# Kernel tuning notes

Hardware: AMD Instinct MI355X
Metric: run time of the kernel (lower is better)

Reference implementation:

```python
import jax, jax.numpy as jnp
import numpy as np
import math

DIM_V = 512
NUM_HEADS = 8
LN_EPS = 1e-5


def _layer_norm(x, g, b):
    mu = jnp.mean(x, axis=-1, keepdims=True)
    var = jnp.mean(jnp.square(x - mu), axis=-1, keepdims=True)
    return (x - mu) * jax.lax.rsqrt(var + LN_EPS) * g + b


def setup_inputs() -> dict:
    key = jax.random.key(0)
    ks = jax.random.split(key, 12)
    B, Nq, Nk, Dq, Dk, Dv = 16, 1024, 1024, 512, 512, DIM_V
    s_q = 1.0 / math.sqrt(Dq)
    s_k = 1.0 / math.sqrt(Dk)
    s_v = 1.0 / math.sqrt(Dv)
    return {
        "Q": jax.random.normal(ks[0], (B, Nq, Dq), jnp.float32),
        "K": jax.random.normal(ks[1], (B, Nk, Dk), jnp.float32),
        "Wq": jax.random.normal(ks[2], (Dq, Dv), jnp.float32) * s_q,
        "bq": jnp.zeros((Dv,), jnp.float32),
        "Wk": jax.random.normal(ks[3], (Dk, Dv), jnp.float32) * s_k,
        "bk": jnp.zeros((Dv,), jnp.float32),
        "Wv": jax.random.normal(ks[4], (Dk, Dv), jnp.float32) * s_k,
        "bv": jnp.zeros((Dv,), jnp.float32),
        "Wo": jax.random.normal(ks[5], (Dv, Dv), jnp.float32) * s_v,
        "bo": jnp.zeros((Dv,), jnp.float32),
        "g0": jnp.ones((Dv,), jnp.float32),
        "b0": jnp.zeros((Dv,), jnp.float32),
        "g1": jnp.ones((Dv,), jnp.float32),
        "b1": jnp.zeros((Dv,), jnp.float32),
    }


def reference(Q, K, Wq, bq, Wk, bk, Wv, bv, Wo, bo, g0, b0, g1, b1):
    B, Nq, _ = Q.shape
    H = NUM_HEADS
    hd = DIM_V // H
    Qp = Q @ Wq + bq            # [B, Nq, Dv]
    Kp = K @ Wk + bk            # [B, Nk, Dv]
    Vp = K @ Wv + bv            # [B, Nk, Dv]
    # split heads: [B, N, H, hd]
    Qh = Qp.reshape(B, Nq, H, hd)
    Kh = Kp.reshape(B, -1, H, hd)
    Vh = Vp.reshape(B, -1, H, hd)
    # NOTE: original scales by sqrt(dim_V), not sqrt(head_dim)
    scores = jnp.einsum("bqhd,bkhd->bhqk", Qh, Kh) / math.sqrt(DIM_V)
    A = jax.nn.softmax(scores, axis=-1)          # [B, H, Nq, Nk]
    Oh = Qh + jnp.einsum("bhqk,bkhd->bqhd", A, Vh)  # residual on projected Q
    O = Oh.reshape(B, Nq, DIM_V)
    O = _layer_norm(O, g0, b0)
    O = O + jax.nn.relu(O @ Wo + bo)
    O = _layer_norm(O, g1, b1)
    return O
```

## Files before the change

### kernel.cpp

```cpp
#include <hip/hip_runtime.h>
#include <hip/hip_bf16.h>

typedef float f32x4 __attribute__((ext_vector_type(4)));
typedef float f32x16 __attribute__((ext_vector_type(16)));
typedef __bf16 bf16x8 __attribute__((ext_vector_type(8)));
typedef __bf16 bf16x4 __attribute__((ext_vector_type(4)));

#define MFMA(a, b, c) __builtin_amdgcn_mfma_f32_16x16x32_bf16(a, b, c, 0, 0, 0)
#define MFMA32(a, b, c) __builtin_amdgcn_mfma_f32_32x32x16_bf16(a, b, c, 0, 0, 0)
#define AS1 __attribute__((address_space(1)))
#define AS3 __attribute__((address_space(3)))

__device__ __forceinline__ void gload16(const void* g, void* l) {
    __builtin_amdgcn_global_load_lds((const AS1 unsigned int*)g, (AS3 unsigned int*)l, 16, 0, 0);
}

__device__ __forceinline__ unsigned short f2bf(float f) {
    union { float f; unsigned u; } x{f};
    unsigned r = x.u + 0x7FFFu + ((x.u >> 16) & 1u);
    return (unsigned short)(r >> 16);
}
__device__ __forceinline__ float bf2f(unsigned short u) {
    union { unsigned u; float f; } x; x.u = ((unsigned)u) << 16; return x.f;
}
__device__ __forceinline__ unsigned pkbf(float a, float b) {
    union { __bf16 h[2]; unsigned u; } r;
    r.h[0] = (__bf16)a; r.h[1] = (__bf16)b;
    return r.u;
}

__device__ __forceinline__ void softmax_pack(const f32x16& s0, const f32x16& s1,
                                             float& ls, int hi, bf16x8* pf) {
    unsigned We[8], Wf[8];
    #pragma unroll
    for (int g = 0; g < 4; ++g) {
        float e0 = __builtin_amdgcn_exp2f(s0[4 * g + 0]);
        float e1 = __builtin_amdgcn_exp2f(s0[4 * g + 1]);
        float e2 = __builtin_amdgcn_exp2f(s0[4 * g + 2]);
        float e3 = __builtin_amdgcn_exp2f(s0[4 * g + 3]);
        float f0 = __builtin_amdgcn_exp2f(s1[4 * g + 0]);
        float f1 = __builtin_amdgcn_exp2f(s1[4 * g + 1]);
        float f2 = __builtin_amdgcn_exp2f(s1[4 * g + 2]);
        float f3 = __builtin_amdgcn_exp2f(s1[4 * g + 3]);
        ls += ((e0 + e1) + (e2 + e3)) + ((f0 + f1) + (f2 + f3));
        We[2 * g + 0] = pkbf(e0, e1); We[2 * g + 1] = pkbf(e2, e3);
        Wf[2 * g + 0] = pkbf(f0, f1); Wf[2 * g + 1] = pkbf(f2, f3);
    }
    #pragma unroll
    for (int src = 0; src < 2; ++src) {
        const unsigned* W = src == 0 ? We : Wf;
        #pragma unroll
        for (int k2 = 0; k2 < 2; ++k2) {
            unsigned A0 = W[4 * k2 + 0], A1 = W[4 * k2 + 1];
            unsigned B0 = W[4 * k2 + 2], B1 = W[4 * k2 + 3];
            unsigned cross0 = __shfl_xor(hi ? A0 : B0, 32);
            unsigned cross1 = __shfl_xor(hi ? A1 : B1, 32);
            union { unsigned w[4]; bf16x8 v; } r;
            r.w[0] = hi ? cross0 : A0;
            r.w[1] = hi ? cross1 : A1;
            r.w[2] = hi ? B0 : cross0;
            r.w[3] = hi ? B1 : cross1;
            pf[src * 2 + k2] = r.v;
        }
    }
}

__global__ __launch_bounds__(256) void k_pack4(const float* W0, const float* W1,
                                               const float* W2, const float* W3,
                                               unsigned short* P0, unsigned short* P1,
                                               unsigned short* P2, unsigned short* P3) {
    __shared__ float T[64][65];
    int sel = blockIdx.x >> 6, tile = blockIdx.x & 63;
    const float* W = sel == 0 ? W0 : sel == 1 ? W1 : sel == 2 ? W2 : W3;
    unsigned short* Wp = sel == 0 ? P0 : sel == 1 ? P1 : sel == 2 ? P2 : P3;
    int k0 = (tile >> 3) * 64, n0 = (tile & 7) * 64;
    int tid = threadIdx.x;
    for (int it = 0; it < 16; ++it) {
        int id = it * 256 + tid;
        int r = id >> 6, c = id & 63;
        T[r][c] = W[(k0 + r) * 512 + n0 + c];
    }
    __syncthreads();
    if (sel < 3) {
        #pragma unroll
        for (int cc = 0; cc < 2; ++cc) {
            int ch = cc * 256 + tid;
            int ksl = ch >> 8, n16l = (ch >> 6) & 3, ln = ch & 63;
            int kg = ln >> 4, nl = ln & 15;
            union { unsigned short u[8]; int4 v; } tmp;
            #pragma unroll
            for (int e = 0; e < 8; ++e)
                tmp.u[e] = f2bf(T[ksl * 32 + kg * 8 + e][n16l * 16 + nl]);
            size_t dst = ((size_t)((k0 >> 5) + ksl) * 32 + (n0 >> 4) + n16l) * 512 + ln * 8;
            *(int4*)(Wp + dst) = tmp.v;
        }
    } else {
        for (int it = 0; it < 16; ++it) {
            int id = it * 256 + tid;
            int r = id >> 6, c = id & 63;
            Wp[(n0 + r) * 512 + k0 + c] = f2bf(T[c][r]);
        }
    }
}

__global__ __launch_bounds__(512, 4) void k_proj3(const float* __restrict__ Qf,
                                                  const float* __restrict__ Kf,
                                                  const unsigned short* __restrict__ WpQ,
                                                  const unsigned short* __restrict__ WpK,
                                                  const unsigned short* __restrict__ WpV,
                                                  const float* __restrict__ bq,
                                                  const float* __restrict__ bk,
                                                  const float* __restrict__ bv,
                                                  unsigned short* __restrict__ Qsc,
                                                  unsigned short* __restrict__ Kp,
                                                  unsigned short* __restrict__ VpT,
                                                  float scale2) {
    __shared__ __align__(16) unsigned short Asm[2][2048];
    const int tid = threadIdx.x, lane = tid & 63, w = tid >> 6;
    const int l15 = lane & 15, l4 = lane >> 4;
    const int bid = blockIdx.x;
    const int sel = bid >> 8, rt = bid & 255;
    const float* A = sel == 0 ? Qf : Kf;
    const unsigned short* Wp = sel == 0 ? WpQ : sel == 1 ? WpK : WpV;
    const int m0 = rt * 64;
    const int wn = w * 64;

    const f32x4 vz = {0.f, 0.f, 0.f, 0.f};
    f32x4 acc[4][4];
    for (int i = 0; i < 4; ++i)
        for (int j = 0; j < 4; ++j) acc[i][j] = vz;

    const int sr = tid >> 3, sc4 = tid & 7;
    const float* aptr = A + (size_t)(m0 + sr) * 512 + sc4 * 4;
    unsigned short* const wdst =
        &Asm[0][0] + sr * 32 + ((sc4 >> 1) ^ (sr & 3)) * 8 + (sc4 & 1) * 4;

    auto WRITEA = [&](const float4& v, int p) {
        union { unsigned u[2]; } r;
        r.u[0] = pkbf(v.x, v.y);
        r.u[1] = pkbf(v.z, v.w);
        *(uint2*)(wdst + p * 2048) = *(uint2*)&r;
    };

    {
        float4 a0 = *(const float4*)(aptr);
        WRITEA(a0, 0);
    }
    __syncthreads();

    const unsigned short* wbase = Wp + (size_t)(w * 4) * 512 + lane * 8;
    if (sel < 2) {
        for (int ks = 0; ks < 16; ++ks) {
            int p = ks & 1;
            float4 anx;
            if (ks < 15) anx = *(const float4*)(aptr + (ks + 1) * 32);
            bf16x8 bfr[4], afr[4];
            #pragma unroll
            for (int j = 0; j < 4; ++j)
                bfr[j] = *(const bf16x8*)(wbase + (size_t)ks * 16384 + j * 512);
            #pragma unroll
            for (int i = 0; i < 4; ++i) {
                int rr = i * 16 + l15;
                afr[i] = *(const bf16x8*)&Asm[p][rr * 32 + (l4 ^ (rr & 3)) * 8];
            }
            __builtin_amdgcn_s_setprio(1);
            #pragma unroll
            for (int i = 0; i < 4; ++i)
                #pragma unroll
                for (int j = 0; j < 4; ++j)
                    acc[i][j] = MFMA(afr[i], bfr[j], acc[i][j]);
            __builtin_amdgcn_s_setprio(0);
            if (ks < 15) WRITEA(anx, p ^ 1);
            __syncthreads();
        }
        const float* bias = sel ? bk : bq;
        unsigned short* out = sel ? Kp : Qsc;
        const float scale = sel ? 1.0f : scale2;
        float bn[4];
        #pragma unroll
        for (int j = 0; j < 4; ++j) bn[j] = bias[wn + j * 16 + l15];
        for (int i = 0; i < 4; ++i)
            for (int j = 0; j < 4; ++j)
                for (int rg = 0; rg < 4; ++rg) {
                    int m = m0 + i * 16 + l4 * 4 + rg;
                    int n = wn + j * 16 + l15;
                    out[(size_t)m * 512 + n] = f2bf((acc[i][j][rg] + bn[j]) * scale);
                }
    } else {
        for (int ks = 0; ks < 16; ++ks) {
            int p = ks & 1;
            float4 anx;
            if (ks < 15) anx = *(const float4*)(aptr + (ks + 1) * 32);
            bf16x8 bfr[4], afr[4];
            #pragma unroll
            for (int j = 0; j < 4; ++j)
                bfr[j] = *(const bf16x8*)(wbase + (size_t)ks * 16384 + j * 512);
            #pragma unroll
            for (int i = 0; i < 4; ++i) {
                int rr = i * 16 + l15;
                afr[i] = *(const bf16x8*)&Asm[p][rr * 32 + (l4 ^ (rr & 3)) * 8];
            }
            __builtin_amdgcn_s_setprio(1);
            #pragma unroll
            for (int i = 0; i < 4; ++i)
                #pragma unroll
                for (int j = 0; j < 4; ++j)
                    acc[i][j] = MFMA(bfr[j], afr[i], acc[i][j]);
            __builtin_amdgcn_s_setprio(0);
            if (ks < 15) WRITEA(anx, p ^ 1);
            __syncthreads();
        }
        const int b = m0 >> 10, key0 = m0 & 1023;
        for (int j = 0; j < 4; ++j) {
            float4 bv4 = *(const float4*)(bv + wn + j * 16 + l4 * 4);
            for (int i = 0; i < 4; ++i)
                for (int rg = 0; rg < 4; ++rg) {
                    int d = wn + j * 16 + l4 * 4 + rg;
                    int key = key0 + i * 16 + l15;
                    VpT[((size_t)(b * 512 + d)) * 1024 + key] = f2bf(acc[i][j][rg] + bv4[rg]);
                }
        }
    }
}

__global__ __launch_bounds__(128, 2) void k_attn64(const unsigned short* __restrict__ Qs,
                                                   const unsigned short* __restrict__ Kp,
                                                   const unsigned short* __restrict__ VpT,
                                                   unsigned short* __restrict__ O1b) {
    __shared__ __align__(16) unsigned short sm[16384];
    const int tid = threadIdx.x, lane = tid & 63, w = tid >> 6;
    const int l31 = lane & 31, hi = lane >> 5;
    int i = blockIdx.x;
    const int xcd = i & 7, r2 = i >> 3;
    const int bhl = r2 & 15, qt = r2 >> 4;
    const int bh = xcd * 16 + bhl;
    const int h = bh & 7, b = bh >> 3;
    const int q0 = b * 1024 + qt * 128 + w * 64;
    const int kv0 = (qt * 3 + bhl * 5) & 15;

    const unsigned short* Ksrc = Kp + (size_t)(b * 1024) * 512 + h * 64;
    const unsigned short* Vsrc = VpT + (size_t)(b * 512 + h * 64) * 1024;
    const unsigned short* qptrA = Qs + (size_t)(q0 + l31) * 512 + h * 64;
    const unsigned short* qptrB = qptrA + (size_t)32 * 512;

    bf16x8 qfA[4], qfB[4];
    #pragma unroll
    for (int ks = 0; ks < 4; ++ks) {
        qfA[ks] = *(const bf16x8*)(qptrA + ks * 16 + hi * 8);
        qfB[ks] = *(const bf16x8*)(qptrB + ks * 16 + hi * 8);
    }

    f32x16 accA0, accA1, accB0, accB1;
    #pragma unroll
    for (int r = 0; r < 16; ++r) { accA0[r] = 0.f; accA1[r] = 0.f; accB0[r] = 0.f; accB1[r] = 0.f; }
    float lsA = 0.f, lsB = 0.f;

    auto STAGE = [&](int j, int p) {
        int t = (j + kv0) & 15;
        #pragma unroll
        for (int it = 0; it < 4; ++it) {
            int id = it * 128 + tid;
            int r = id >> 3, x = id & 7, c = x ^ (r & 7);
            unsigned short* kb = sm + p * 4096 + (it * 128 + w * 64) * 8;
            gload16(Ksrc + (size_t)(t * 64 + r) * 512 + c * 8, kb);
            gload16(Vsrc + (size_t)r * 1024 + t * 64 + c * 8, kb + 8192);
        }
    };

    STAGE(0, 0);
    __syncthreads();
    const int rsw = l31 & 7;
    for (int it2 = 0; it2 < 16; ++it2) {
        int p = it2 & 1;
        if (it2 < 15) STAGE(it2 + 1, p ^ 1);
        const unsigned short* Kl = sm + p * 4096;
        const unsigned short* Vl = sm + 8192 + p * 4096;

        f32x16 s0a, s1a, s0b, s1b;
        #pragma unroll
        for (int r = 0; r < 16; ++r) { s0a[r] = 0.f; s1a[r] = 0.f; s0b[r] = 0.f; s1b[r] = 0.f; }
        __builtin_amdgcn_s_setprio(1);
        #pragma unroll
        for (int ks = 0; ks < 4; ++ks) {
            int c = (2 * ks + hi) ^ rsw;
            bf16x8 kf0 = *(const bf16x8*)&Kl[l31 * 64 + c * 8];
            bf16x8 kf1 = *(const bf16x8*)&Kl[(32 + l31) * 64 + c * 8];
            s0a = MFMA32(kf0, qfA[ks], s0a);
            s1a = MFMA32(kf1, qfA[ks], s1a);
            s0b = MFMA32(kf0, qfB[ks], s0b);
            s1b = MFMA32(kf1, qfB[ks], s1b);
        }
        __builtin_amdgcn_s_setprio(0);

        bf16x8 pfA[4], pfB[4];
        softmax_pack(s0a, s1a, lsA, hi, pfA);
        softmax_pack(s0b, s1b, lsB, hi, pfB);

        __builtin_amdgcn_s_setprio(1);
        #pragma unroll
        for (int ks = 0; ks < 4; ++ks) {
            int c = (2 * ks + hi) ^ rsw;
            bf16x8 vf0 = *(const bf16x8*)&Vl[l31 * 64 + c * 8];
            bf16x8 vf1 = *(const bf16x8*)&Vl[(32 + l31) * 64 + c * 8];
            accA0 = MFMA32(vf0, pfA[ks], accA0);
            accA1 = MFMA32(vf1, pfA[ks], accA1);
            accB0 = MFMA32(vf0, pfB[ks], accB0);
            accB1 = MFMA32(vf1, pfB[ks], accB1);
        }
        __builtin_amdgcn_s_setprio(0);
        __syncthreads();
    }

    const float invscale = 15.6841306f;
    {
        float l = lsA + __shfl_xor(lsA, 32);
        float linv = 1.0f / l;
        unsigned short* orow = O1b + (size_t)(q0 + l31) * 512 + h * 64;
        #pragma unroll
        for (int g = 0; g < 4; ++g) {
            int d0 = 8 * g + 4 * hi;
            bf16x4 qres = *(const bf16x4*)(qptrA + d0);
            bf16x4 ov;
            for (int j = 0; j < 4; ++j)
                ov[j] = (__bf16)((float)qres[j] * invscale + accA0[4 * g + j] * linv);
            *(bf16x4*)(orow + d0) = ov;
            int d1 = 32 + d0;
            bf16x4 qres1 = *(const bf16x4*)(qptrA + d1);
            bf16x4 ov1;
            for (int j = 0; j < 4; ++j)
                ov1[j] = (__bf16)((float)qres1[j] * invscale + accA1[4 * g + j] * linv);
            *(bf16x4*)(orow + d1) = ov1;
        }
    }
    {
        float l = lsB + __shfl_xor(lsB, 32);
        float linv = 1.0f / l;
        unsigned short* orow = O1b + (size_t)(q0 + 32 + l31) * 512 + h * 64;
        #pragma unroll
        for (int g = 0; g < 4; ++g) {
            int d0 = 8 * g + 4 * hi;
            bf16x4 qres = *(const bf16x4*)(qptrB + d0);
            bf16x4 ov;
            for (int j = 0; j < 4; ++j)
                ov[j] = (__bf16)((float)qres[j] * invscale + accB0[4 * g + j] * linv);
            *(bf16x4*)(orow + d0) = ov;
            int d1 = 32 + d0;
            bf16x4 qres1 = *(const bf16x4*)(qptrB + d1);
            bf16x4 ov1;
            for (int j = 0; j < 4; ++j)
                ov1[j] = (__bf16)((float)qres1[j] * invscale + accB1[4 * g + j] * linv);
            *(bf16x4*)(orow + d1) = ov1;
        }
    }
}

__global__ __launch_bounds__(256) void k_ln_bf(const unsigned short* __restrict__ in,
                                               unsigned short* __restrict__ outb,
                                               const float* __restrict__ g,
                                               const float* __restrict__ bt) {
    int row = blockIdx.x * 4 + (threadIdx.x >> 6);
    int lane = threadIdx.x & 63;
    const unsigned short* x = in + (size_t)row * 512 + lane * 8;
    bf16x8 v = *(const bf16x8*)x;
    float f[8];
    for (int j = 0; j < 8; ++j) f[j] = (float)v[j];
    float s1 = 0.f, s2 = 0.f;
    for (int j = 0; j < 8; ++j) { s1 += f[j]; s2 += f[j] * f[j]; }
    for (int off = 32; off; off >>= 1) {
        s1 += __shfl_xor(s1, off);
        s2 += __shfl_xor(s2, off);
    }
    float mu = s1 * (1.f / 512.f);
    float var = s2 * (1.f / 512.f) - mu * mu;
    float rs = rsqrtf(var + 1e-5f);
    float4 ga = *(const float4*)(g + lane * 8), gb = *(const float4*)(g + lane * 8 + 4);
    float4 ba = *(const float4*)(bt + lane * 8), bb = *(const float4*)(bt + lane * 8 + 4);
    float gg[8] = {ga.x, ga.y, ga.z, ga.w, gb.x, gb.y, gb.z, gb.w};
    float bv[8] = {ba.x, ba.y, ba.z, ba.w, bb.x, bb.y, bb.z, bb.w};
    bf16x8 y;
    for (int j = 0; j < 8; ++j) y[j] = (__bf16)((f[j] - mu) * rs * gg[j] + bv[j]);
    *(bf16x8*)(outb + (size_t)row * 512 + lane * 8) = y;
}

__global__ __launch_bounds__(512, 2) void k_gemm2ln(const unsigned short* __restrict__ A,
                                                    const unsigned short* __restrict__ Bt,
                                                    const float* __restrict__ bias,
                                                    const float* __restrict__ g1,
                                                    const float* __restrict__ b1,
                                                    float* __restrict__ out) {
    __shared__ __align__(16) unsigned short Ab[2][2048];
    __shared__ __align__(16) unsigned short Bb[2][16384];
    __shared__ float part[64][4][2];
    __shared__ float stats[64][2];
    const int tid = threadIdx.x, lane = tid & 63, w = tid >> 6;
    const int l15 = lane & 15, l4 = lane >> 4;
    const int m0 = blockIdx.x * 64;
    const int wm = (w >> 2) * 32, wn = (w & 3) * 128;

    const f32x4 vz = {0.f, 0.f, 0.f, 0.f};
    f32x4 acc[2][8];
    for (int i = 0; i < 2; ++i)
        for (int j = 0; j < 8; ++j) acc[i][j] = vz;

    const unsigned short* Abase = A + (size_t)m0 * 512;

    auto STAGE = [&](int ks, int p) {
        int kk = ks * 32;
        for (int it = 0; it < 4; ++it) {
            int id = it * 512 + tid;
            int r = id >> 2, x = id & 3, c = x ^ (r & 3);
            gload16(Bt + r * 512 + kk + c * 8, &Bb[p][(it * 512 + w * 64) * 8]);
        }
        if (w < 4) {
            int id = w * 64 + lane;
            int r = id >> 2, x = id & 3, c = x ^ (r & 3);
            gload16(Abase + r * 512 + kk + c * 8, &Ab[p][(w * 64) * 8]);
        }
    };

    STAGE(0, 0);
    __syncthreads();
    for (int ks = 0; ks < 16; ++ks) {
        int p = ks & 1;
        if (ks < 15) STAGE(ks + 1, p ^ 1);
        bf16x8 af[2], bfr[8];
        for (int i = 0; i < 2; ++i) {
            int r = wm + i * 16 + l15, pc = l4 ^ (r & 3);
            af[i] = *(const bf16x8*)&Ab[p][r * 32 + pc * 8];
        }
        for (int j = 0; j < 8; ++j) {
            int r = wn + j * 16 + l15, pc = l4 ^ (r & 3);
            bfr[j] = *(const bf16x8*)&Bb[p][r * 32 + pc * 8];
        }
        __builtin_amdgcn_s_setprio(1);
        for (int i = 0; i < 2; ++i)
            for (int j = 0; j < 8; ++j)
                acc[i][j] = MFMA(af[i], bfr[j], acc[i][j]);
        __builtin_amdgcn_s_setprio(0);
        __syncthreads();
    }

    float bn[8], gv[8], bv2[8];
    for (int j = 0; j < 8; ++j) {
        int n = wn + j * 16 + l15;
        bn[j] = bias[n]; gv[j] = g1[n]; bv2[j] = b1[n];
    }
    f32x4 s1v[2], s2v[2];
    for (int i = 0; i < 2; ++i) { s1v[i] = vz; s2v[i] = vz; }
    for (int i = 0; i < 2; ++i)
        for (int j = 0; j < 8; ++j)
            for (int rg = 0; rg < 4; ++rg) {
                int row = m0 + wm + i * 16 + l4 * 4 + rg;
                int n = wn + j * 16 + l15;
                float z = acc[i][j][rg] + bn[j];
                z = z > 0.f ? z : 0.f;
                float v = bf2f(A[(size_t)row * 512 + n]) + z;
                acc[i][j][rg] = v;
                s1v[i][rg] += v;
                s2v[i][rg] += v * v;
            }
    for (int i = 0; i < 2; ++i)
        for (int rg = 0; rg < 4; ++rg) {
            float a = s1v[i][rg], c = s2v[i][rg];
            for (int off = 1; off < 16; off <<= 1) {
                a += __shfl_xor(a, off);
                c += __shfl_xor(c, off);
            }
            s1v[i][rg] = a; s2v[i][rg] = c;
        }
    if (l15 == 0)
        for (int i = 0; i < 2; ++i)
            for (int rg = 0; rg < 4; ++rg) {
                int rl = wm + i * 16 + l4 * 4 + rg;
                part[rl][w & 3][0] = s1v[i][rg];
                part[rl][w & 3][1] = s2v[i][rg];
            }
    __syncthreads();
    if (tid < 64) {
        float a = 0.f, c = 0.f;
        for (int q = 0; q < 4; ++q) { a += part[tid][q][0]; c += part[tid][q][1]; }
        float mu = a * (1.f / 512.f);
        float var = c * (1.f / 512.f) - mu * mu;
        stats[tid][0] = mu;
        stats[tid][1] = rsqrtf(var + 1e-5f);
    }
    __syncthreads();
    for (int i = 0; i < 2; ++i)
        for (int rg = 0; rg < 4; ++rg) {
            int rl = wm + i * 16 + l4 * 4 + rg;
            float mu = stats[rl][0], rs = stats[rl][1];
            for (int j = 0; j < 8; ++j) {
                int n = wn + j * 16 + l15;
                out[(size_t)(m0 + rl) * 512 + n] = (acc[i][j][rg] - mu) * rs * gv[j] + bv2[j];
            }
        }
}

extern "C" void kernel_launch(void* const* d_in, const int* in_sizes, int n_in,
                              void* d_out, int out_size, void* d_ws, size_t ws_size,
                              hipStream_t stream) {
    const float* Q  = (const float*)d_in[0];
    const float* K  = (const float*)d_in[1];
    const float* Wq = (const float*)d_in[2];
    const float* bq = (const float*)d_in[3];
    const float* Wk = (const float*)d_in[4];
    const float* bk = (const float*)d_in[5];
    const float* Wv = (const float*)d_in[6];
    const float* bv = (const float*)d_in[7];
    const float* Wo = (const float*)d_in[8];
    const float* bo = (const float*)d_in[9];
    const float* g0 = (const float*)d_in[10];
    const float* b0 = (const float*)d_in[11];
    const float* g1 = (const float*)d_in[12];
    const float* b1 = (const float*)d_in[13];
    float* out = (float*)d_out;

    const size_t SZ_BF = (size_t)16384 * 512 * 2;
    const size_t SZ_W  = (size_t)512 * 512 * 2;
    char* p = (char*)d_ws;
    unsigned short* WpQ = (unsigned short*)p; p += SZ_W;
    unsigned short* WpK = (unsigned short*)p; p += SZ_W;
    unsigned short* WpV = (unsigned short*)p; p += SZ_W;
    unsigned short* Wot = (unsigned short*)p; p += SZ_W;
    unsigned short* Qsc = (unsigned short*)p; p += SZ_BF;
    unsigned short* Kp  = (unsigned short*)p; p += SZ_BF;
    unsigned short* VpT = (unsigned short*)p; p += SZ_BF;
    unsigned short* A1b = (unsigned short*)p; p += SZ_BF;
    unsigned short* X0b = (unsigned short*)p; p += SZ_BF;

    k_pack4<<<256, 256, 0, stream>>>(Wq, Wk, Wv, Wo, WpQ, WpK, WpV, Wot);

    const float scale2 = 0.063758718f;
    k_proj3<<<768, 512, 0, stream>>>(Q, K, WpQ, WpK, WpV, bq, bk, bv, Qsc, Kp, VpT, scale2);

    k_attn64<<<1024, 128, 0, stream>>>(Qsc, Kp, VpT, A1b);

    k_ln_bf<<<4096, 256, 0, stream>>>(A1b, X0b, g0, b0);
    k_gemm2ln<<<256, 512, 0, stream>>>(X0b, Wot, bo, g1, b1, out);
}
```

Measured before the change: 144.0 us.

## Replace two-wave attention blocks with single-wave blocks using 32-key tiles and waitcnt pipelining

The attention kernel moves from 128-thread blocks (two waves sharing 64-key K/V tiles) to 64-thread single-wave blocks that each stage 32-key K/V tiles in 16KB of LDS. Since only one wave touches the shared buffers, __syncthreads is replaced by explicit s_waitcnt vmcnt/lgkmcnt fences, and softmax packing is cut down to one 32-wide score tile. This removes block barriers and allows more independent resident blocks per CU. In exchange, K/V staging is no longer shared between two waves, which doubles global/L2 traffic per query, and iterations are shorter with less MFMA work to hide latency.

```diff
diff --git a/kernel.cpp b/kernel.cpp
--- a/kernel.cpp
+++ b/kernel.cpp
@@ -29,39 +29,30 @@
     return r.u;
 }
 
-__device__ __forceinline__ void softmax_pack(const f32x16& s0, const f32x16& s1,
-                                             float& ls, int hi, bf16x8* pf) {
-    unsigned We[8], Wf[8];
+__device__ __forceinline__ void softmax_pack32(const f32x16& s, float& ls, int hi, bf16x8* pf) {
+    unsigned W[8];
     #pragma unroll
     for (int g = 0; g < 4; ++g) {
-        float e0 = __builtin_amdgcn_exp2f(s0[4 * g + 0]);
-        float e1 = __builtin_amdgcn_exp2f(s0[4 * g + 1]);
-        float e2 = __builtin_amdgcn_exp2f(s0[4 * g + 2]);
-        float e3 = __builtin_amdgcn_exp2f(s0[4 * g + 3]);
-        float f0 = __builtin_amdgcn_exp2f(s1[4 * g + 0]);
-        float f1 = __builtin_amdgcn_exp2f(s1[4 * g + 1]);
-        float f2 = __builtin_amdgcn_exp2f(s1[4 * g + 2]);
-        float f3 = __builtin_amdgcn_exp2f(s1[4 * g + 3]);
-        ls += ((e0 + e1) + (e2 + e3)) + ((f0 + f1) + (f2 + f3));
-        We[2 * g + 0] = pkbf(e0, e1); We[2 * g + 1] = pkbf(e2, e3);
-        Wf[2 * g + 0] = pkbf(f0, f1); Wf[2 * g + 1] = pkbf(f2, f3);
+        float e0 = __builtin_amdgcn_exp2f(s[4 * g + 0]);
+        float e1 = __builtin_amdgcn_exp2f(s[4 * g + 1]);
+        float e2 = __builtin_amdgcn_exp2f(s[4 * g + 2]);
+        float e3 = __builtin_amdgcn_exp2f(s[4 * g + 3]);
+        ls += (e0 + e1) + (e2 + e3);
+        W[2 * g + 0] = pkbf(e0, e1);
+        W[2 * g + 1] = pkbf(e2, e3);
     }
     #pragma unroll
-    for (int src = 0; src < 2; ++src) {
-        const unsigned* W = src == 0 ? We : Wf;
-        #pragma unroll
-        for (int k2 = 0; k2 < 2; ++k2) {
-            unsigned A0 = W[4 * k2 + 0], A1 = W[4 * k2 + 1];
-            unsigned B0 = W[4 * k2 + 2], B1 = W[4 * k2 + 3];
-            unsigned cross0 = __shfl_xor(hi ? A0 : B0, 32);
-            unsigned cross1 = __shfl_xor(hi ? A1 : B1, 32);
-            union { unsigned w[4]; bf16x8 v; } r;
-            r.w[0] = hi ? cross0 : A0;
-            r.w[1] = hi ? cross1 : A1;
-            r.w[2] = hi ? B0 : cross0;
-            r.w[3] = hi ? B1 : cross1;
-            pf[src * 2 + k2] = r.v;
-        }
+    for (int k2 = 0; k2 < 2; ++k2) {
+        unsigned A0 = W[4 * k2 + 0], A1 = W[4 * k2 + 1];
+        unsigned B0 = W[4 * k2 + 2], B1 = W[4 * k2 + 3];
+        unsigned c0 = __shfl_xor(hi ? A0 : B0, 32);
+        unsigned c1 = __shfl_xor(hi ? A1 : B1, 32);
+        union { unsigned w[4]; bf16x8 v; } r;
+        r.w[0] = hi ? c0 : A0;
+        r.w[1] = hi ? c1 : A1;
+        r.w[2] = hi ? B0 : c0;
+        r.w[3] = hi ? B1 : c1;
+        pf[k2] = r.v;
     }
 }
 
@@ -223,20 +214,20 @@
     }
 }
 
-__global__ __launch_bounds__(128, 2) void k_attn64(const unsigned short* __restrict__ Qs,
-                                                   const unsigned short* __restrict__ Kp,
-                                                   const unsigned short* __restrict__ VpT,
-                                                   unsigned short* __restrict__ O1b) {
-    __shared__ __align__(16) unsigned short sm[16384];
-    const int tid = threadIdx.x, lane = tid & 63, w = tid >> 6;
+__global__ __launch_bounds__(64) void k_attn1w(const unsigned short* __restrict__ Qs,
+                                               const unsigned short* __restrict__ Kp,
+                                               const unsigned short* __restrict__ VpT,
+                                               unsigned short* __restrict__ O1b) {
+    __shared__ __align__(16) unsigned short sm[8192];
+    const int lane = threadIdx.x;
     const int l31 = lane & 31, hi = lane >> 5;
     int i = blockIdx.x;
-    const int xcd = i & 7, r2 = i >> 3;
-    const int bhl = r2 & 15, qt = r2 >> 4;
+    const int xcd = i & 7, loc = i >> 3;
+    const int bhl = loc & 15, qt = loc >> 4;
     const int bh = xcd * 16 + bhl;
     const int h = bh & 7, b = bh >> 3;
-    const int q0 = b * 1024 + qt * 128 + w * 64;
-    const int kv0 = (qt * 3 + bhl * 5) & 15;
+    const int q0 = b * 1024 + qt * 64;
+    const int kv0 = (bhl * 5 + qt * 3) & 31;
 
     const unsigned short* Ksrc = Kp + (size_t)(b * 1024) * 512 + h * 64;
     const unsigned short* Vsrc = VpT + (size_t)(b * 512 + h * 64) * 1024;
@@ -255,60 +246,64 @@
     for (int r = 0; r < 16; ++r) { accA0[r] = 0.f; accA1[r] = 0.f; accB0[r] = 0.f; accB1[r] = 0.f; }
     float lsA = 0.f, lsB = 0.f;
 
-    auto STAGE = [&](int j, int p) {
-        int t = (j + kv0) & 15;
-        #pragma unroll
-        for (int it = 0; it < 4; ++it) {
-            int id = it * 128 + tid;
-            int r = id >> 3, x = id & 7, c = x ^ (r & 7);
-            unsigned short* kb = sm + p * 4096 + (it * 128 + w * 64) * 8;
-            gload16(Ksrc + (size_t)(t * 64 + r) * 512 + c * 8, kb);
-            gload16(Vsrc + (size_t)r * 1024 + t * 64 + c * 8, kb + 8192);
-        }
+    const int krow = lane >> 3;
+    const int kg = (lane & 7) ^ krow;
+    const int vrow = lane >> 2;
+    const int vg = (lane & 3) ^ (vrow & 3);
+
+    auto STAGE = [&](int tp, int p) {
+        #pragma unroll
+        for (int c = 0; c < 4; ++c)
+            gload16(Ksrc + (size_t)(tp * 32 + c * 8 + krow) * 512 + kg * 8,
+                    sm + p * 4096 + c * 512);
+        #pragma unroll
+        for (int c = 0; c < 4; ++c)
+            gload16(Vsrc + (size_t)(c * 16 + vrow) * 1024 + tp * 32 + vg * 8,
+                    sm + p * 4096 + 2048 + c * 512);
     };
 
-    STAGE(0, 0);
-    __syncthreads();
-    const int rsw = l31 & 7;
-    for (int it2 = 0; it2 < 16; ++it2) {
-        int p = it2 & 1;
-        if (it2 < 15) STAGE(it2 + 1, p ^ 1);
+    STAGE(kv0, 0);
+    for (int t = 0; t < 32; ++t) {
+        int p = t & 1;
+        asm volatile("s_waitcnt lgkmcnt(0)" ::: "memory");
+        if (t < 31) {
+            STAGE((t + 1 + kv0) & 31, p ^ 1);
+            asm volatile("s_waitcnt vmcnt(8)" ::: "memory");
+        } else {
+            asm volatile("s_waitcnt vmcnt(0)" ::: "memory");
+        }
         const unsigned short* Kl = sm + p * 4096;
-        const unsigned short* Vl = sm + 8192 + p * 4096;
-
-        f32x16 s0a, s1a, s0b, s1b;
-        #pragma unroll
-        for (int r = 0; r < 16; ++r) { s0a[r] = 0.f; s1a[r] = 0.f; s0b[r] = 0.f; s1b[r] = 0.f; }
+        const unsigned short* Vl = sm + p * 4096 + 2048;
+
+        f32x16 sa, sb;
+        #pragma unroll
+        for (int r = 0; r < 16; ++r) { sa[r] = 0.f; sb[r] = 0.f; }
         __builtin_amdgcn_s_setprio(1);
         #pragma unroll
         for (int ks = 0; ks < 4; ++ks) {
-            int c = (2 * ks + hi) ^ rsw;
-            bf16x8 kf0 = *(const bf16x8*)&Kl[l31 * 64 + c * 8];
-            bf16x8 kf1 = *(const bf16x8*)&Kl[(32 + l31) * 64 + c * 8];
-            s0a = MFMA32(kf0, qfA[ks], s0a);
-            s1a = MFMA32(kf1, qfA[ks], s1a);
-            s0b = MFMA32(kf0, qfB[ks], s0b);
-            s1b = MFMA32(kf1, qfB[ks], s1b);
+            int gq = (2 * ks + hi) ^ (l31 & 7);
+            bf16x8 kf = *(const bf16x8*)&Kl[l31 * 64 + gq * 8];
+            sa = MFMA32(kf, qfA[ks], sa);
+            sb = MFMA32(kf, qfB[ks], sb);
         }
         __builtin_amdgcn_s_setprio(0);
 
-        bf16x8 pfA[4], pfB[4];
-        softmax_pack(s0a, s1a, lsA, hi, pfA);
-        softmax_pack(s0b, s1b, lsB, hi, pfB);
+        bf16x8 pfA[2], pfB[2];
+        softmax_pack32(sa, lsA, hi, pfA);
+        softmax_pack32(sb, lsB, hi, pfB);
 
         __builtin_amdgcn_s_setprio(1);
         #pragma unroll
-        for (int ks = 0; ks < 4; ++ks) {
-            int c = (2 * ks + hi) ^ rsw;
-            bf16x8 vf0 = *(const bf16x8*)&Vl[l31 * 64 + c * 8];
-            bf16x8 vf1 = *(const bf16x8*)&Vl[(32 + l31) * 64 + c * 8];
-            accA0 = MFMA32(vf0, pfA[ks], accA0);
-            accA1 = MFMA32(vf1, pfA[ks], accA1);
-            accB0 = MFMA32(vf0, pfB[ks], accB0);
-            accB1 = MFMA32(vf1, pfB[ks], accB1);
+        for (int k2 = 0; k2 < 2; ++k2) {
+            int gv = (2 * k2 + hi) ^ (l31 & 3);
+            bf16x8 vf0 = *(const bf16x8*)&Vl[l31 * 32 + gv * 8];
+            bf16x8 vf1 = *(const bf16x8*)&Vl[(32 + l31) * 32 + gv * 8];
+            accA0 = MFMA32(vf0, pfA[k2], accA0);
+            accA1 = MFMA32(vf1, pfA[k2], accA1);
+            accB0 = MFMA32(vf0, pfB[k2], accB0);
+            accB1 = MFMA32(vf1, pfB[k2], accB1);
         }
         __builtin_amdgcn_s_setprio(0);
-        __syncthreads();
     }
 
     const float invscale = 15.6841306f;
@@ -533,7 +528,7 @@
     const float scale2 = 0.063758718f;
     k_proj3<<<768, 512, 0, stream>>>(Q, K, WpQ, WpK, WpV, bq, bk, bv, Qsc, Kp, VpT, scale2);
 
-    k_attn64<<<1024, 128, 0, stream>>>(Qsc, Kp, VpT, A1b);
+    k_attn1w<<<2048, 64, 0, stream>>>(Qsc, Kp, VpT, A1b);
 
     k_ln_bf<<<4096, 256, 0, stream>>>(A1b, X0b, g0, b0);
     k_gemm2ln<<<256, 512, 0, stream>>>(X0b, Wot, bo, g1, b1, out);
```

Result: slower. 155.6 us (+8.1%).

## Restructure attention to 4 waves of 32 query rows per block

Applied to the files above, without the earlier changes.

The attention kernel now runs 256 threads per block, with each wave handling 32 query rows instead of 64. This halves per-wave accumulator and score registers, so up to 4 blocks can fit per CU, which should hide latency better. Each block still covers 128 queries, but the K/V tile staged in LDS is now shared by four waves, and the staggered KV start offset per block is dropped. In exchange, each wave does less MFMA work per K/V fragment read from LDS, so LDS read traffic per FLOP doubles.

```diff
diff --git a/kernel.cpp b/kernel.cpp
--- a/kernel.cpp
+++ b/kernel.cpp
@@ -27,42 +27,6 @@
     union { __bf16 h[2]; unsigned u; } r;
     r.h[0] = (__bf16)a; r.h[1] = (__bf16)b;
     return r.u;
-}
-
-__device__ __forceinline__ void softmax_pack(const f32x16& s0, const f32x16& s1,
-                                             float& ls, int hi, bf16x8* pf) {
-    unsigned We[8], Wf[8];
-    #pragma unroll
-    for (int g = 0; g < 4; ++g) {
-        float e0 = __builtin_amdgcn_exp2f(s0[4 * g + 0]);
-        float e1 = __builtin_amdgcn_exp2f(s0[4 * g + 1]);
-        float e2 = __builtin_amdgcn_exp2f(s0[4 * g + 2]);
-        float e3 = __builtin_amdgcn_exp2f(s0[4 * g + 3]);
-        float f0 = __builtin_amdgcn_exp2f(s1[4 * g + 0]);
-        float f1 = __builtin_amdgcn_exp2f(s1[4 * g + 1]);
-        float f2 = __builtin_amdgcn_exp2f(s1[4 * g + 2]);
-        float f3 = __builtin_amdgcn_exp2f(s1[4 * g + 3]);
-        ls += ((e0 + e1) + (e2 + e3)) + ((f0 + f1) + (f2 + f3));
-        We[2 * g + 0] = pkbf(e0, e1); We[2 * g + 1] = pkbf(e2, e3);
-        Wf[2 * g + 0] = pkbf(f0, f1); Wf[2 * g + 1] = pkbf(f2, f3);
-    }
-    #pragma unroll
-    for (int src = 0; src < 2; ++src) {
-        const unsigned* W = src == 0 ? We : Wf;
-        #pragma unroll
-        for (int k2 = 0; k2 < 2; ++k2) {
-            unsigned A0 = W[4 * k2 + 0], A1 = W[4 * k2 + 1];
-            unsigned B0 = W[4 * k2 + 2], B1 = W[4 * k2 + 3];
-            unsigned cross0 = __shfl_xor(hi ? A0 : B0, 32);
-            unsigned cross1 = __shfl_xor(hi ? A1 : B1, 32);
-            union { unsigned w[4]; bf16x8 v; } r;
-            r.w[0] = hi ? cross0 : A0;
-            r.w[1] = hi ? cross1 : A1;
-            r.w[2] = hi ? B0 : cross0;
-            r.w[3] = hi ? B1 : cross1;
-            pf[src * 2 + k2] = r.v;
-        }
-    }
 }
 
 __global__ __launch_bounds__(256) void k_pack4(const float* W0, const float* W1,
@@ -223,7 +187,7 @@
     }
 }
 
-__global__ __launch_bounds__(128, 2) void k_attn64(const unsigned short* __restrict__ Qs,
+__global__ __launch_bounds__(256, 4) void k_attn32(const unsigned short* __restrict__ Qs,
                                                    const unsigned short* __restrict__ Kp,
                                                    const unsigned short* __restrict__ VpT,
                                                    unsigned short* __restrict__ O1b) {
@@ -231,125 +195,132 @@
     const int tid = threadIdx.x, lane = tid & 63, w = tid >> 6;
     const int l31 = lane & 31, hi = lane >> 5;
     int i = blockIdx.x;
-    const int xcd = i & 7, r2 = i >> 3;
-    const int bhl = r2 & 15, qt = r2 >> 4;
+    const int xcd = i & 7, jj = i >> 3;
+    const int qt = jj & 7, bhl = jj >> 3;
     const int bh = xcd * 16 + bhl;
     const int h = bh & 7, b = bh >> 3;
-    const int q0 = b * 1024 + qt * 128 + w * 64;
-    const int kv0 = (qt * 3 + bhl * 5) & 15;
+    const int qrow = b * 1024 + qt * 128 + w * 32 + l31;
 
     const unsigned short* Ksrc = Kp + (size_t)(b * 1024) * 512 + h * 64;
     const unsigned short* Vsrc = VpT + (size_t)(b * 512 + h * 64) * 1024;
-    const unsigned short* qptrA = Qs + (size_t)(q0 + l31) * 512 + h * 64;
-    const unsigned short* qptrB = qptrA + (size_t)32 * 512;
-
-    bf16x8 qfA[4], qfB[4];
+    const unsigned short* qptr = Qs + (size_t)qrow * 512 + h * 64;
+
+    bf16x8 qf[4];
     #pragma unroll
-    for (int ks = 0; ks < 4; ++ks) {
-        qfA[ks] = *(const bf16x8*)(qptrA + ks * 16 + hi * 8);
-        qfB[ks] = *(const bf16x8*)(qptrB + ks * 16 + hi * 8);
-    }
-
-    f32x16 accA0, accA1, accB0, accB1;
+    for (int ks = 0; ks < 4; ++ks)
+        qf[ks] = *(const bf16x8*)(qptr + ks * 16 + hi * 8);
+
+    f32x16 acc0, acc1;
     #pragma unroll
-    for (int r = 0; r < 16; ++r) { accA0[r] = 0.f; accA1[r] = 0.f; accB0[r] = 0.f; accB1[r] = 0.f; }
-    float lsA = 0.f, lsB = 0.f;
-
-    auto STAGE = [&](int j, int p) {
-        int t = (j + kv0) & 15;
-        #pragma unroll
-        for (int it = 0; it < 4; ++it) {
-            int id = it * 128 + tid;
+    for (int r = 0; r < 16; ++r) { acc0[r] = 0.f; acc1[r] = 0.f; }
+    float ls = 0.f;
+
+    auto STAGE = [&](int kv, int p) {
+        #pragma unroll
+        for (int it = 0; it < 2; ++it) {
+            int id = it * 256 + tid;
             int r = id >> 3, x = id & 7, c = x ^ (r & 7);
-            unsigned short* kb = sm + p * 4096 + (it * 128 + w * 64) * 8;
-            gload16(Ksrc + (size_t)(t * 64 + r) * 512 + c * 8, kb);
-            gload16(Vsrc + (size_t)r * 1024 + t * 64 + c * 8, kb + 8192);
+            unsigned short* ldsb = sm + p * 4096 + (it * 256 + w * 64) * 8;
+            gload16(Ksrc + (size_t)(kv * 64 + r) * 512 + c * 8, ldsb);
+            gload16(Vsrc + (size_t)r * 1024 + kv * 64 + c * 8, ldsb + 8192);
         }
     };
 
     STAGE(0, 0);
     __syncthreads();
-    const int rsw = l31 & 7;
-    for (int it2 = 0; it2 < 16; ++it2) {
-        int p = it2 & 1;
-        if (it2 < 15) STAGE(it2 + 1, p ^ 1);
+    for (int kv = 0; kv < 16; ++kv) {
+        int p = kv & 1;
+        if (kv < 15) STAGE(kv + 1, p ^ 1);
         const unsigned short* Kl = sm + p * 4096;
         const unsigned short* Vl = sm + 8192 + p * 4096;
-
-        f32x16 s0a, s1a, s0b, s1b;
-        #pragma unroll
-        for (int r = 0; r < 16; ++r) { s0a[r] = 0.f; s1a[r] = 0.f; s0b[r] = 0.f; s1b[r] = 0.f; }
+        const int rsw = (l31 & 7);
+
+        f32x16 s0, s1;
+        #pragma unroll
+        for (int r = 0; r < 16; ++r) { s0[r] = 0.f; s1[r] = 0.f; }
         __builtin_amdgcn_s_setprio(1);
         #pragma unroll
         for (int ks = 0; ks < 4; ++ks) {
             int c = (2 * ks + hi) ^ rsw;
             bf16x8 kf0 = *(const bf16x8*)&Kl[l31 * 64 + c * 8];
+            s0 = MFMA32(kf0, qf[ks], s0);
             bf16x8 kf1 = *(const bf16x8*)&Kl[(32 + l31) * 64 + c * 8];
-            s0a = MFMA32(kf0, qfA[ks], s0a);
-            s1a = MFMA32(kf1, qfA[ks], s1a);
-            s0b = MFMA32(kf0, qfB[ks], s0b);
-            s1b = MFMA32(kf1, qfB[ks], s1b);
+            s1 = MFMA32(kf1, qf[ks], s1);
         }
         __builtin_amdgcn_s_setprio(0);
 
-        bf16x8 pfA[4], pfB[4];
-        softmax_pack(s0a, s1a, lsA, hi, pfA);
-        softmax_pack(s0b, s1b, lsB, hi, pfB);
+        unsigned We[8], Wf[8];
+        #pragma unroll
+        for (int g = 0; g < 4; ++g) {
+            float e0 = __builtin_amdgcn_exp2f(s0[4 * g + 0]);
+            float e1 = __builtin_amdgcn_exp2f(s0[4 * g + 1]);
+            float e2 = __builtin_amdgcn_exp2f(s0[4 * g + 2]);
+            float e3 = __builtin_amdgcn_exp2f(s0[4 * g + 3]);
+            float f0 = __builtin_amdgcn_exp2f(s1[4 * g + 0]);
+            float f1 = __builtin_amdgcn_exp2f(s1[4 * g + 1]);
+            float f2 = __builtin_amdgcn_exp2f(s1[4 * g + 2]);
+            float f3 = __builtin_amdgcn_exp2f(s1[4 * g + 3]);
+            ls += ((e0 + e1) + (e2 + e3)) + ((f0 + f1) + (f2 + f3));
+            We[2 * g + 0] = pkbf(e0, e1); We[2 * g + 1] = pkbf(e2, e3);
+            Wf[2 * g + 0] = pkbf(f0, f1); Wf[2 * g + 1] = pkbf(f2, f3);
+        }
+        bf16x8 pf[4];
+        #pragma unroll
+        for (int src = 0; src < 2; ++src) {
+            const unsigned* W = src == 0 ? We : Wf;
+            #pragma unroll
+            for (int k2 = 0; k2 < 2; ++k2) {
+                unsigned A0 = W[4 * k2 + 0], A1 = W[4 * k2 + 1];
+                unsigned B0 = W[4 * k2 + 2], B1 = W[4 * k2 + 3];
+                unsigned cross0 = __shfl_xor(hi ? A0 : B0, 32);
+                unsigned cross1 = __shfl_xor(hi ? A1 : B1, 32);
+                union { unsigned w[4]; bf16x8 v; } r;
+                r.w[0] = hi ? cross0 : A0;
+                r.w[1] = hi ? cross1 : A1;
+                r.w[2] = hi ? B0 : cross0;
+                r.w[3] = hi ? B1 : cross1;
+                pf[src * 2 + k2] = r.v;
+            }
+        }
 
         __builtin_amdgcn_s_setprio(1);
         #pragma unroll
         for (int ks = 0; ks < 4; ++ks) {
             int c = (2 * ks + hi) ^ rsw;
             bf16x8 vf0 = *(const bf16x8*)&Vl[l31 * 64 + c * 8];
+            acc0 = MFMA32(vf0, pf[ks], acc0);
             bf16x8 vf1 = *(const bf16x8*)&Vl[(32 + l31) * 64 + c * 8];
-            accA0 = MFMA32(vf0, pfA[ks], accA0);
-            accA1 = MFMA32(vf1, pfA[ks], accA1);
-            accB0 = MFMA32(vf0, pfB[ks], accB0);
-            accB1 = MFMA32(vf1, pfB[ks], accB1);
+            acc1 = MFMA32(vf1, pf[ks], acc1);
         }
         __builtin_amdgcn_s_setprio(0);
         __syncthreads();
     }
 
+    ls += __shfl_xor(ls, 32);
+    float linv = 1.0f / ls;
     const float invscale = 15.6841306f;
-    {
-        float l = lsA + __shfl_xor(lsA, 32);
-        float linv = 1.0f / l;
-        unsigned short* orow = O1b + (size_t)(q0 + l31) * 512 + h * 64;
-        #pragma unroll
-        for (int g = 0; g < 4; ++g) {
+    unsigned short* orow = O1b + (size_t)qrow * 512 + h * 64;
+    #pragma unroll
+    for (int g = 0; g < 4; ++g) {
+        {
             int d0 = 8 * g + 4 * hi;
-            bf16x4 qres = *(const bf16x4*)(qptrA + d0);
+            bf16x4 qres = *(const bf16x4*)(qptr + d0);
             bf16x4 ov;
-            for (int j = 0; j < 4; ++j)
-                ov[j] = (__bf16)((float)qres[j] * invscale + accA0[4 * g + j] * linv);
+            ov[0] = (__bf16)((float)qres[0] * invscale + acc0[4 * g + 0] * linv);
+            ov[1] = (__bf16)((float)qres[1] * invscale + acc0[4 * g + 1] * linv);
+            ov[2] = (__bf16)((float)qres[2] * invscale + acc0[4 * g + 2] * linv);
+            ov[3] = (__bf16)((float)qres[3] * invscale + acc0[4 * g + 3] * linv);
             *(bf16x4*)(orow + d0) = ov;
-            int d1 = 32 + d0;
-            bf16x4 qres1 = *(const bf16x4*)(qptrA + d1);
-            bf16x4 ov1;
-            for (int j = 0; j < 4; ++j)
-                ov1[j] = (__bf16)((float)qres1[j] * invscale + accA1[4 * g + j] * linv);
-            *(bf16x4*)(orow + d1) = ov1;
-        }
-    }
-    {
-        float l = lsB + __shfl_xor(lsB, 32);
-        float linv = 1.0f / l;
-        unsigned short* orow = O1b + (size_t)(q0 + 32 + l31) * 512 + h * 64;
-        #pragma unroll
-        for (int g = 0; g < 4; ++g) {
-            int d0 = 8 * g + 4 * hi;
-            bf16x4 qres = *(const bf16x4*)(qptrB + d0);
+        }
+        {
+            int d0 = 32 + 8 * g + 4 * hi;
+            bf16x4 qres = *(const bf16x4*)(qptr + d0);
             bf16x4 ov;
-            for (int j = 0; j < 4; ++j)
-                ov[j] = (__bf16)((float)qres[j] * invscale + accB0[4 * g + j] * linv);
+            ov[0] = (__bf16)((float)qres[0] * invscale + acc1[4 * g + 0] * linv);
+            ov[1] = (__bf16)((float)qres[1] * invscale + acc1[4 * g + 1] * linv);
+            ov[2] = (__bf16)((float)qres[2] * invscale + acc1[4 * g + 2] * linv);
+            ov[3] = (__bf16)((float)qres[3] * invscale + acc1[4 * g + 3] * linv);
             *(bf16x4*)(orow + d0) = ov;
-            int d1 = 32 + d0;
-            bf16x4 qres1 = *(const bf16x4*)(qptrB + d1);
-            bf16x4 ov1;
-            for (int j = 0; j < 4; ++j)
-                ov1[j] = (__bf16)((float)qres1[j] * invscale + accB1[4 * g + j] * linv);
-            *(bf16x4*)(orow + d1) = ov1;
         }
     }
 }
@@ -533,7 +504,7 @@
     const float scale2 = 0.063758718f;
     k_proj3<<<768, 512, 0, stream>>>(Q, K, WpQ, WpK, WpV, bq, bk, bv, Qsc, Kp, VpT, scale2);
 
-    k_attn64<<<1024, 128, 0, stream>>>(Qsc, Kp, VpT, A1b);
+    k_attn32<<<1024, 256, 0, stream>>>(Qsc, Kp, VpT, A1b);
 
     k_ln_bf<<<4096, 256, 0, stream>>>(A1b, X0b, g0, b0);
     k_gemm2ln<<<256, 512, 0, stream>>>(X0b, Wot, bo, g1, b1, out);
```

Measured after the change: 143.3 us, median of 2. No clear change (-0.5%).
